# Optimization experiments

Measured on AMD Instinct MI355X. Metric: run time of the kernel, lower is better.

## Reference

```python
import jax, jax.numpy as jnp
import numpy as np

N_ATOMS = 200_000
N_BONDS = 400_000
DEG = 2            # each bond receives from exactly 2 atoms (a2b edges)
D = 128


def setup_inputs() -> dict:
    key = jax.random.key(0)
    k1, k2, k3 = jax.random.split(key, 3)
    atom_ft = jax.random.normal(k1, (N_ATOMS, D), dtype=jnp.float32)
    bond_ft = jax.random.normal(k2, (N_BONDS, D), dtype=jnp.float32)
    edge_src = jax.random.randint(k3, (N_BONDS * DEG,), 0, N_ATOMS, dtype=jnp.int32)
    # every bond has exactly DEG incoming a2b edges -> dst is sorted repeats
    edge_dst = jnp.repeat(jnp.arange(N_BONDS, dtype=jnp.int32), DEG)
    return {"atom_ft": atom_ft, "bond_ft": bond_ft,
            "edge_src": edge_src, "edge_dst": edge_dst}


def reference(atom_ft, bond_ft, edge_src, edge_dst):
    """copy_u gather -> per-dst-segment mean and max -> concat with dst feats."""
    n_bonds = bond_ft.shape[0]
    msgs = atom_ft[edge_src]                                        # [E, D] gather
    seg_sum = jax.ops.segment_sum(msgs, edge_dst, num_segments=n_bonds)   # [n_bonds, D]
    cnt = jax.ops.segment_sum(jnp.ones((msgs.shape[0],), msgs.dtype),
                              edge_dst, num_segments=n_bonds)             # [n_bonds]
    mean_v = seg_sum / jnp.maximum(cnt, 1.0)[:, None]
    max_v = jax.ops.segment_max(msgs, edge_dst, num_segments=n_bonds)
    max_v = jnp.where(cnt[:, None] > 0, max_v, 0.0)  # guard empty segments
    return jnp.concatenate((bond_ft, mean_v, max_v), axis=1)        # [n_bonds, 3D]
```

## Files before the change

### kernel.cpp

```cpp
#include <hip/hip_runtime.h>


#define D      128
#define OUT_D  (3 * D)
#define BPG    4
#define THREADS 256

typedef float vfloat4 __attribute__((ext_vector_type(4)));

__global__ __launch_bounds__(THREADS, 4) void concat_mean_max_kernel(
    const float* __restrict__ atom_ft,
    const float* __restrict__ bond_ft,
    const int*  __restrict__ edge_src,
    float* __restrict__ out,
    int n_bonds)
{
    const int lane   = threadIdx.x & 31;
    const int grp    = blockIdx.x * (THREADS >> 5) + (threadIdx.x >> 5);
    const int ngrp   = gridDim.x * (THREADS >> 5);
    const int stride = ngrp * BPG;

    int base = grp * BPG;
    if (base >= n_bonds) return;

    int s[2 * BPG];
#pragma unroll
    for (int j = 0; j < BPG; ++j) {
        int b  = base + j;
        int bb = (b < n_bonds) ? b : (n_bonds - 1);
        s[2 * j]     = edge_src[2 * bb];
        s[2 * j + 1] = edge_src[2 * bb + 1];
    }

    while (true) {
        vfloat4 v0[BPG], v1[BPG], bf[BPG];
        int bb[BPG];
#pragma unroll
        for (int j = 0; j < BPG; ++j) {
            int b = base + j;
            bb[j] = (b < n_bonds) ? b : (n_bonds - 1);
            v0[j] = ((const vfloat4*)(atom_ft + (size_t)s[2 * j]     * D))[lane];
            v1[j] = ((const vfloat4*)(atom_ft + (size_t)s[2 * j + 1] * D))[lane];
            bf[j] = __builtin_nontemporal_load(
                        ((const vfloat4*)(bond_ft + (size_t)bb[j] * D)) + lane);
        }

        const int next = base + stride;
        if (next < n_bonds) {
#pragma unroll
            for (int j = 0; j < BPG; ++j) {
                int b  = next + j;
                int nb = (b < n_bonds) ? b : (n_bonds - 1);
                s[2 * j]     = edge_src[2 * nb];
                s[2 * j + 1] = edge_src[2 * nb + 1];
            }
        }

#pragma unroll
        for (int j = 0; j < BPG; ++j) {
            vfloat4 mean = (v0[j] + v1[j]) * 0.5f;
            vfloat4 mx;
            mx.x = fmaxf(v0[j].x, v1[j].x);
            mx.y = fmaxf(v0[j].y, v1[j].y);
            mx.z = fmaxf(v0[j].z, v1[j].z);
            mx.w = fmaxf(v0[j].w, v1[j].w);

            vfloat4* orow = (vfloat4*)(out + (size_t)bb[j] * OUT_D);
            __builtin_nontemporal_store(bf[j], orow + lane);
            __builtin_nontemporal_store(mean,  orow + 32 + lane);
            __builtin_nontemporal_store(mx,    orow + 64 + lane);
        }

        base = next;
        if (base >= n_bonds) break;
    }
}

extern "C" void kernel_launch(void* const* d_in, const int* in_sizes, int n_in,
                              void* d_out, int out_size, void* d_ws, size_t ws_size,
                              hipStream_t stream) {
    const float* atom_ft  = (const float*)d_in[0];
    const float* bond_ft  = (const float*)d_in[1];
    const int*   edge_src = (const int*)d_in[2];
    float* out = (float*)d_out;

    const int n_bonds = in_sizes[1] / D;

    const int groups_needed = (n_bonds + BPG - 1) / BPG;
    const int blocks_full   = (groups_needed + (THREADS >> 5) - 1) / (THREADS >> 5);
    const int blocks        = blocks_full < 2048 ? blocks_full : 2048;

    concat_mean_max_kernel<<<blocks, THREADS, 0, stream>>>(
        atom_ft, bond_ft, edge_src, out, n_bonds);
}
```

Before: 794.2 us.

## Split bond copy into separate streaming kernel and widen gather grid

Moves the bond_ft-to-output copy out of the gather kernel into its own fully coalesced streaming kernel that runs first. The gather kernel then only loads atom rows and writes the mean and max slices, and its grid cap is raised from 2048 to 4096 blocks. The aim is to make the gather loop lighter and give it more parallelism to hide random-gather latency. The cost is a second kernel launch and two passes that each write partial output rows, which can lose locality in partially written cache lines.

```diff
diff --git a/kernel.cpp b/kernel.cpp
--- a/kernel.cpp
+++ b/kernel.cpp
@@ -8,9 +8,37 @@
 
 typedef float vfloat4 __attribute__((ext_vector_type(4)));
 
-__global__ __launch_bounds__(THREADS, 4) void concat_mean_max_kernel(
+__global__ __launch_bounds__(THREADS, 8) void copy_bond_kernel(
+    const float* __restrict__ bond_ft,
+    float* __restrict__ out,
+    int n_bonds)
+{
+    const int total  = n_bonds * 32;
+    const int stride = gridDim.x * THREADS;
+    int i = blockIdx.x * THREADS + threadIdx.x;
+
+    const vfloat4* __restrict__ src = (const vfloat4*)bond_ft;
+    vfloat4* __restrict__ dst = (vfloat4*)out;
+
+    for (; i + 3 * stride < total; i += 4 * stride) {
+        const int e0 = i, e1 = i + stride, e2 = i + 2 * stride, e3 = i + 3 * stride;
+        vfloat4 a = __builtin_nontemporal_load(src + e0);
+        vfloat4 b = __builtin_nontemporal_load(src + e1);
+        vfloat4 c = __builtin_nontemporal_load(src + e2);
+        vfloat4 d = __builtin_nontemporal_load(src + e3);
+        __builtin_nontemporal_store(a, dst + ((e0 >> 5) * 96 + (e0 & 31)));
+        __builtin_nontemporal_store(b, dst + ((e1 >> 5) * 96 + (e1 & 31)));
+        __builtin_nontemporal_store(c, dst + ((e2 >> 5) * 96 + (e2 & 31)));
+        __builtin_nontemporal_store(d, dst + ((e3 >> 5) * 96 + (e3 & 31)));
+    }
+    for (; i < total; i += stride) {
+        vfloat4 a = __builtin_nontemporal_load(src + i);
+        __builtin_nontemporal_store(a, dst + ((i >> 5) * 96 + (i & 31)));
+    }
+}
+
+__global__ __launch_bounds__(THREADS, 4) void gather_mean_max_kernel(
     const float* __restrict__ atom_ft,
-    const float* __restrict__ bond_ft,
     const int*  __restrict__ edge_src,
     float* __restrict__ out,
     int n_bonds)
@@ -33,7 +61,7 @@
     }
 
     while (true) {
-        vfloat4 v0[BPG], v1[BPG], bf[BPG];
+        vfloat4 v0[BPG], v1[BPG];
         int bb[BPG];
 #pragma unroll
         for (int j = 0; j < BPG; ++j) {
@@ -41,8 +69,6 @@
             bb[j] = (b < n_bonds) ? b : (n_bonds - 1);
             v0[j] = ((const vfloat4*)(atom_ft + (size_t)s[2 * j]     * D))[lane];
             v1[j] = ((const vfloat4*)(atom_ft + (size_t)s[2 * j + 1] * D))[lane];
-            bf[j] = __builtin_nontemporal_load(
-                        ((const vfloat4*)(bond_ft + (size_t)bb[j] * D)) + lane);
         }
 
         const int next = base + stride;
@@ -66,9 +92,8 @@
             mx.w = fmaxf(v0[j].w, v1[j].w);
 
             vfloat4* orow = (vfloat4*)(out + (size_t)bb[j] * OUT_D);
-            __builtin_nontemporal_store(bf[j], orow + lane);
-            __builtin_nontemporal_store(mean,  orow + 32 + lane);
-            __builtin_nontemporal_store(mx,    orow + 64 + lane);
+            __builtin_nontemporal_store(mean, orow + 32 + lane);
+            __builtin_nontemporal_store(mx,   orow + 64 + lane);
         }
 
         base = next;
@@ -86,10 +111,12 @@
 
     const int n_bonds = in_sizes[1] / D;
 
+    copy_bond_kernel<<<2048, THREADS, 0, stream>>>(bond_ft, out, n_bonds);
+
     const int groups_needed = (n_bonds + BPG - 1) / BPG;
     const int blocks_full   = (groups_needed + (THREADS >> 5) - 1) / (THREADS >> 5);
-    const int blocks        = blocks_full < 2048 ? blocks_full : 2048;
+    const int blocks        = blocks_full < 4096 ? blocks_full : 4096;
 
-    concat_mean_max_kernel<<<blocks, THREADS, 0, stream>>>(
-        atom_ft, bond_ft, edge_src, out, n_bonds);
+    gather_mean_max_kernel<<<blocks, THREADS, 0, stream>>>(
+        atom_ft, edge_src, out, n_bonds);
 }
```

After: 825.8 us. 1.04x slower.
